# Optimization experiments

Measured on AMD Instinct MI355X. Metric: run time of the kernel, lower is better.

Reference implementation:

```python
import jax, jax.numpy as jnp
import numpy as np

DIM = 1024
NUM_HEADS = 16
HEAD_DIM = DIM // NUM_HEADS


def setup_inputs() -> dict:
    key = jax.random.key(0)
    k_x, k_wqkv, k_bqkv, k_wo, k_bo = jax.random.split(key, 5)
    scale = DIM ** -0.5
    return {
        "x": jax.random.normal(k_x, (4, 2048, DIM), dtype=jnp.float32),
        "w_qkv": jax.random.normal(k_wqkv, (DIM, 3 * DIM), dtype=jnp.float32) * scale,
        "b_qkv": jax.random.normal(k_bqkv, (3 * DIM,), dtype=jnp.float32) * 0.02,
        "w_out": jax.random.normal(k_wo, (DIM, DIM), dtype=jnp.float32) * scale,
        "b_out": jax.random.normal(k_bo, (DIM,), dtype=jnp.float32) * 0.02,
    }


def reference(x, w_qkv, b_qkv, w_out, b_out):
    B, S, D = x.shape
    H, Hd = NUM_HEADS, HEAD_DIM
    # QKV projection: (B,S,3D) -> (3,B,H,S,Hd)
    qkv = (x @ w_qkv + b_qkv).reshape(B, S, 3, H, Hd).transpose(2, 0, 3, 1, 4)
    q, k, v = qkv[0], qkv[1], qkv[2]
    scores = jnp.einsum('bhqd,bhkd->bhqk', q, k) / (Hd ** 0.5)
    attn = jax.nn.softmax(scores, axis=-1)  # dropout is identity in eval
    out = jnp.einsum('bhqk,bhkd->bhqd', attn, v)
    out = out.transpose(0, 2, 1, 3).reshape(B, S, D)
    return out @ w_out + b_out
```

## Files before the change

### kernel.cpp

```cpp
#include <hip/hip_runtime.h>
#include <hip/hip_bf16.h>
#include <stdint.h>

#define SEQ 2048
#define DIM 1024
#define NH 16
#define HD 64

typedef __attribute__((ext_vector_type(8))) short short8;
typedef __attribute__((ext_vector_type(4))) float f32x4;
typedef __attribute__((ext_vector_type(4))) float float4v;
typedef __attribute__((ext_vector_type(4))) unsigned short u16x4;
typedef __attribute__((ext_vector_type(2))) unsigned int u32x2;

#define MFMA16(a, b, c) __builtin_amdgcn_mfma_f32_16x16x32_bf16(a, b, c, 0, 0, 0)

__device__ __forceinline__ unsigned short f2b(float f) {
  union { float f; unsigned int u; } x; x.f = f;
  unsigned int r = (x.u + 0x7FFFu + ((x.u >> 16) & 1u)) >> 16;
  return (unsigned short)r;
}

__device__ __forceinline__ unsigned int pk2(float a, float b) {
  __hip_bfloat162 h = __float22bfloat162_rn(float2{a, b});
  union { __hip_bfloat162 h; unsigned int u; } c; c.h = h;
  return c.u;
}

__device__ __forceinline__ void gld16(const void* g, void* l) {
  __builtin_amdgcn_global_load_lds(
      (const __attribute__((address_space(1))) unsigned int*)(uintptr_t)g,
      (__attribute__((address_space(3))) unsigned int*)(unsigned int)(uintptr_t)l,
      16, 0, 0);
}

__global__ void cast_bf16_kernel(const float* __restrict__ in,
                                 unsigned short* __restrict__ out, int n4) {
  int stride = gridDim.x * blockDim.x;
  for (int i = blockIdx.x * blockDim.x + threadIdx.x; i < n4; i += stride) {
    float4v v = *(const float4v*)(in + (size_t)i * 4);
    u16x4 o;
    o.x = f2b(v.x); o.y = f2b(v.y); o.z = f2b(v.z); o.w = f2b(v.w);
    *(u16x4*)(out + (size_t)i * 4) = o;
  }
}

__global__ void transpose_cast_kernel(const float* __restrict__ in,
                                      unsigned short* __restrict__ out,
                                      int rows, int cols) {
  __shared__ float tile[32][33];
  const int t = threadIdx.x, tx = t & 31, ty = t >> 5;
  const int c0 = blockIdx.x * 32, r0 = blockIdx.y * 32;
#pragma unroll
  for (int j = 0; j < 4; j++)
    tile[ty + 8 * j][tx] = in[(size_t)(r0 + ty + 8 * j) * cols + c0 + tx];
  __syncthreads();
#pragma unroll
  for (int j = 0; j < 4; j++)
    out[(size_t)(c0 + ty + 8 * j) * rows + r0 + tx] = f2b(tile[tx][ty + 8 * j]);
}

template <int EPI>
__global__ __launch_bounds__(256, 2) void gemm_bt_kernel(
    const unsigned short* __restrict__ A, const unsigned short* __restrict__ Bt,
    const float* __restrict__ bias, float* __restrict__ Cf,
    int M, int N, int K,
    unsigned short* __restrict__ Qb, unsigned short* __restrict__ Kb,
    unsigned short* __restrict__ Vt) {
  __shared__ unsigned short lA[128 * 32];
  __shared__ unsigned short lB[128 * 32];
  const int t = threadIdx.x, lane = t & 63, w = t >> 6;
  const int l15 = lane & 15, lg = lane >> 4;
  const int wr = (w >> 1) * 64, wc = (w & 1) * 64;
  const int bm = blockIdx.x, bn = blockIdx.y;
  const char* Ag = (const char*)(A + (size_t)bm * 128 * K);
  const char* Bg = (const char*)(Bt + (size_t)bn * 128 * K);
  const int sr = t >> 2;
  const int sc = (t & 3) * 16;
  const size_t rowb = (size_t)K * 2;

  f32x4 acc[4][4];
#pragma unroll
  for (int m = 0; m < 4; m++)
#pragma unroll
    for (int n = 0; n < 4; n++) acc[m][n] = (f32x4){0.f, 0.f, 0.f, 0.f};

  for (int k0 = 0; k0 < K; k0 += 32) {
    __syncthreads();
    const size_t kbyte = (size_t)k0 * 2;
    gld16(Ag + (size_t)sr * rowb + kbyte + sc, &lA[t * 8]);
    gld16(Ag + (size_t)(sr + 64) * rowb + kbyte + sc, &lA[2048 + t * 8]);
    gld16(Bg + (size_t)sr * rowb + kbyte + sc, &lB[t * 8]);
    gld16(Bg + (size_t)(sr + 64) * rowb + kbyte + sc, &lB[2048 + t * 8]);
    asm volatile("s_waitcnt vmcnt(0)" ::: "memory");
    __syncthreads();
    short8 af[4], bf_[4];
#pragma unroll
    for (int m = 0; m < 4; m++)
      af[m] = *(const short8*)&lA[(wr + m * 16 + l15) * 32 + lg * 8];
#pragma unroll
    for (int n = 0; n < 4; n++)
      bf_[n] = *(const short8*)&lB[(wc + n * 16 + l15) * 32 + lg * 8];
#pragma unroll
    for (int m = 0; m < 4; m++)
#pragma unroll
      for (int n = 0; n < 4; n++)
        acc[m][n] = MFMA16(af[m], bf_[n], acc[m][n]);
  }

#pragma unroll
  for (int m = 0; m < 4; m++) {
#pragma unroll
    for (int n = 0; n < 4; n++) {
      const int row0 = bm * 128 + wr + m * 16 + lg * 4;
      const int col = bn * 128 + wc + n * 16 + l15;
      const float bv = bias[col];
#pragma unroll
      for (int rr = 0; rr < 4; rr++) {
        const float v = acc[m][n][rr] + bv;
        const int row = row0 + rr;
        if (EPI == 1) {
          Cf[(size_t)row * N + col] = v;
        } else {
          const int three = col >> 10, rem = col & 1023;
          const int h = rem >> 6, d = rem & 63;
          const int b = row >> 11, s = row & 2047;
          const size_t bh = (size_t)(b * NH + h);
          if (three == 0)
            Qb[(bh * SEQ + s) * HD + d] = f2b(v * 0.125f);
          else if (three == 1)
            Kb[(bh * SEQ + s) * HD + d] = f2b(v);
          else
            Vt[(bh * HD + d) * SEQ + s] = f2b(v);
        }
      }
    }
  }
}

__global__ __launch_bounds__(256, 4) void attn_kernel(
    const unsigned short* __restrict__ Qb, const unsigned short* __restrict__ Kb,
    const unsigned short* __restrict__ Vt, unsigned short* __restrict__ AO) {
  __shared__ unsigned short kT[2][64 * 64];
  __shared__ unsigned short vT[2][64 * 64];
  __shared__ unsigned short pT[4][16 * 64];
  const int t = threadIdx.x, lane = t & 63, w = t >> 6;
  const int l15 = lane & 15, lg = lane >> 4;
  const int q0 = blockIdx.x * 64;
  const int bh = blockIdx.y;
  const char* Qg = (const char*)(Qb + (size_t)bh * SEQ * HD);
  const char* Kg = (const char*)(Kb + (size_t)bh * SEQ * HD);
  const char* Vg = (const char*)(Vt + (size_t)bh * HD * SEQ);

  short8 qa[2];
  {
    const char* qrow = Qg + (size_t)(q0 + w * 16 + l15) * 128;
    qa[0] = *(const short8*)(qrow + lg * 16);
    qa[1] = *(const short8*)(qrow + 64 + lg * 16);
  }

  f32x4 o[4];
#pragma unroll
  for (int n = 0; n < 4; n++) o[n] = (f32x4){0.f, 0.f, 0.f, 0.f};
  float m_r = -1e30f, l_r = 0.f;

  const int sr0 = t >> 3;
  const int scx = (t & 7) * 16;

#define STAGE(buf, kv0_)                                                               \
  do {                                                                                 \
    const int r0_ = sr0, r1_ = sr0 + 32;                                               \
    gld16(Kg + (size_t)((kv0_) + r0_) * 128 + (scx ^ ((r0_ & 7) << 4)),                \
          &kT[buf][t * 8]);                                                            \
    gld16(Kg + (size_t)((kv0_) + r1_) * 128 + (scx ^ ((r1_ & 7) << 4)),                \
          &kT[buf][2048 + t * 8]);                                                     \
    gld16(Vg + (size_t)r0_ * (SEQ * 2) + (size_t)(kv0_) * 2 + (scx ^ ((r0_ & 7) << 4)),\
          &vT[buf][t * 8]);                                                            \
    gld16(Vg + (size_t)r1_ * (SEQ * 2) + (size_t)(kv0_) * 2 + (scx ^ ((r1_ & 7) << 4)),\
          &vT[buf][2048 + t * 8]);                                                     \
  } while (0)

  STAGE(0, 0);
  asm volatile("s_waitcnt vmcnt(0)" ::: "memory");
  __syncthreads();
  int cur = 0;

  for (int kv0 = 0; kv0 < SEQ; kv0 += 64) {
    if (kv0 + 64 < SEQ) STAGE(cur ^ 1, kv0 + 64);

    const unsigned short* kb = &kT[cur][0];
    f32x4 s[4];
#pragma unroll
    for (int n = 0; n < 4; n++) s[n] = (f32x4){0.f, 0.f, 0.f, 0.f};
    __builtin_amdgcn_s_setprio(1);
#pragma unroll
    for (int n = 0; n < 4; n++) {
      const int row = n * 16 + l15;
      const char* kr = (const char*)kb + row * 128;
      const int sw = (row & 7) << 4;
      short8 a0 = *(const short8*)(kr + ((lg * 16) ^ sw));
      short8 a1 = *(const short8*)(kr + ((64 + lg * 16) ^ sw));
      s[n] = MFMA16(a0, qa[0], s[n]);
      s[n] = MFMA16(a1, qa[1], s[n]);
    }
    __builtin_amdgcn_s_setprio(0);

    float mx = s[0][0];
#pragma unroll
    for (int n = 0; n < 4; n++)
#pragma unroll
      for (int r = 0; r < 4; r++) mx = fmaxf(mx, s[n][r]);
    mx = fmaxf(mx, __shfl_xor(mx, 16, 64));
    mx = fmaxf(mx, __shfl_xor(mx, 32, 64));
    const float nm = fmaxf(m_r, mx);
    const float al = __expf(m_r - nm);
    m_r = nm;
    float rs = 0.f;
#pragma unroll
    for (int n = 0; n < 4; n++)
#pragma unroll
      for (int r = 0; r < 4; r++) {
        const float p = __expf(s[n][r] - nm);
        s[n][r] = p;
        rs += p;
      }
    rs += __shfl_xor(rs, 16, 64);
    rs += __shfl_xor(rs, 32, 64);
    l_r = l_r * al + rs;

    float alb[4];
#pragma unroll
    for (int r = 0; r < 4; r++) alb[r] = __shfl(al, lg * 4 + r, 64);
#pragma unroll
    for (int n = 0; n < 4; n++)
#pragma unroll
      for (int r = 0; r < 4; r++) o[n][r] *= alb[r];

    char* pb = (char*)&pT[w][0];
    const int swp = (l15 & 7) << 4;
#pragma unroll
    for (int n = 0; n < 4; n++) {
      u32x2 c;
      c.x = pk2(s[n][0], s[n][1]);
      c.y = pk2(s[n][2], s[n][3]);
      *(u32x2*)(pb + l15 * 128 + ((n * 32 + lg * 8) ^ swp)) = c;
    }
    short8 pa[2];
    pa[0] = *(const short8*)(pb + l15 * 128 + ((lg * 16) ^ swp));
    pa[1] = *(const short8*)(pb + l15 * 128 + ((64 + lg * 16) ^ swp));

    const unsigned short* vb = &vT[cur][0];
    __builtin_amdgcn_s_setprio(1);
#pragma unroll
    for (int n = 0; n < 4; n++) {
      const int row = n * 16 + l15;
      const char* vr = (const char*)vb + row * 128;
      const int sw = (row & 7) << 4;
      short8 b0 = *(const short8*)(vr + ((lg * 16) ^ sw));
      short8 b1 = *(const short8*)(vr + ((64 + lg * 16) ^ sw));
      o[n] = MFMA16(pa[0], b0, o[n]);
      o[n] = MFMA16(pa[1], b1, o[n]);
    }
    __builtin_amdgcn_s_setprio(0);

    asm volatile("s_waitcnt vmcnt(0)" ::: "memory");
    __syncthreads();
    cur ^= 1;
  }
#undef STAGE

  float lb[4];
#pragma unroll
  for (int r = 0; r < 4; r++) lb[r] = 1.f / __shfl(l_r, lg * 4 + r, 64);
  const int b = bh >> 4, h = bh & 15;
  unsigned short* aob = AO + (size_t)b * SEQ * DIM + (size_t)h * HD;
#pragma unroll
  for (int n = 0; n < 4; n++)
#pragma unroll
    for (int r = 0; r < 4; r++) {
      const int s_ = q0 + w * 16 + lg * 4 + r;
      const int d_ = n * 16 + l15;
      aob[(size_t)s_ * DIM + d_] = f2b(o[n][r] * lb[r]);
    }
}

extern "C" void kernel_launch(void* const* d_in, const int* in_sizes, int n_in,
                              void* d_out, int out_size, void* d_ws, size_t ws_size,
                              hipStream_t stream) {
  const float* x = (const float*)d_in[0];
  const float* w_qkv = (const float*)d_in[1];
  const float* b_qkv = (const float*)d_in[2];
  const float* w_out = (const float*)d_in[3];
  const float* b_out = (const float*)d_in[4];
  float* out = (float*)d_out;

  char* ws = (char*)d_ws;
  unsigned short* xb    = (unsigned short*)(ws);
  unsigned short* wqkvT = (unsigned short*)(ws + (16u << 20));
  unsigned short* woT   = (unsigned short*)(ws + (22u << 20));
  unsigned short* Qb    = (unsigned short*)(ws + (24u << 20));
  unsigned short* Kb    = (unsigned short*)(ws + (40u << 20));
  unsigned short* Vt    = (unsigned short*)(ws + (56u << 20));
  unsigned short* AO    = (unsigned short*)(ws + (72u << 20));

  const int M = 4 * SEQ;

  cast_bf16_kernel<<<2048, 256, 0, stream>>>(x, xb, M * DIM / 4);
  transpose_cast_kernel<<<dim3(3 * DIM / 32, DIM / 32), 256, 0, stream>>>(w_qkv, wqkvT, DIM, 3 * DIM);
  transpose_cast_kernel<<<dim3(DIM / 32, DIM / 32), 256, 0, stream>>>(w_out, woT, DIM, DIM);

  gemm_bt_kernel<0><<<dim3(M / 128, 3 * DIM / 128), 256, 0, stream>>>(
      xb, wqkvT, b_qkv, nullptr, M, 3 * DIM, DIM, Qb, Kb, Vt);

  attn_kernel<<<dim3(SEQ / 64, 4 * NH), 256, 0, stream>>>(Qb, Kb, Vt, AO);

  gemm_bt_kernel<1><<<dim3(M / 128, DIM / 128), 256, 0, stream>>>(
      AO, woT, b_out, out, M, DIM, DIM, nullptr, nullptr, nullptr);
}
```

Before: 332.2 us.

## Process two query tiles per wave and use lazy exp2 softmax rescaling

```diff
diff --git a/kernel.cpp b/kernel.cpp
--- a/kernel.cpp
+++ b/kernel.cpp
@@ -14,6 +14,9 @@
 typedef __attribute__((ext_vector_type(2))) unsigned int u32x2;
 
 #define MFMA16(a, b, c) __builtin_amdgcn_mfma_f32_16x16x32_bf16(a, b, c, 0, 0, 0)
+
+#define QSCALE 0.1803368801111244f
+#define LOG2_THR 11.0f
 
 __device__ __forceinline__ unsigned short f2b(float f) {
   union { float f; unsigned int u; } x; x.f = f;
@@ -127,7 +130,7 @@
           const int b = row >> 11, s = row & 2047;
           const size_t bh = (size_t)(b * NH + h);
           if (three == 0)
-            Qb[(bh * SEQ + s) * HD + d] = f2b(v * 0.125f);
+            Qb[(bh * SEQ + s) * HD + d] = f2b(v * QSCALE);
           else if (three == 1)
             Kb[(bh * SEQ + s) * HD + d] = f2b(v);
           else
@@ -138,31 +141,34 @@
   }
 }
 
-__global__ __launch_bounds__(256, 4) void attn_kernel(
+__global__ __launch_bounds__(256, 3) void attn_kernel(
     const unsigned short* __restrict__ Qb, const unsigned short* __restrict__ Kb,
     const unsigned short* __restrict__ Vt, unsigned short* __restrict__ AO) {
   __shared__ unsigned short kT[2][64 * 64];
   __shared__ unsigned short vT[2][64 * 64];
-  __shared__ unsigned short pT[4][16 * 64];
+  __shared__ unsigned short pT[4][32 * 64];
   const int t = threadIdx.x, lane = t & 63, w = t >> 6;
   const int l15 = lane & 15, lg = lane >> 4;
-  const int q0 = blockIdx.x * 64;
+  const int q0 = blockIdx.x * 128;
   const int bh = blockIdx.y;
   const char* Qg = (const char*)(Qb + (size_t)bh * SEQ * HD);
   const char* Kg = (const char*)(Kb + (size_t)bh * SEQ * HD);
   const char* Vg = (const char*)(Vt + (size_t)bh * HD * SEQ);
 
-  short8 qa[2];
-  {
-    const char* qrow = Qg + (size_t)(q0 + w * 16 + l15) * 128;
-    qa[0] = *(const short8*)(qrow + lg * 16);
-    qa[1] = *(const short8*)(qrow + 64 + lg * 16);
-  }
-
-  f32x4 o[4];
-#pragma unroll
-  for (int n = 0; n < 4; n++) o[n] = (f32x4){0.f, 0.f, 0.f, 0.f};
-  float m_r = -1e30f, l_r = 0.f;
+  short8 qa[2][2];
+#pragma unroll
+  for (int h = 0; h < 2; h++) {
+    const char* qrow = Qg + (size_t)(q0 + w * 32 + h * 16 + l15) * 128;
+    qa[h][0] = *(const short8*)(qrow + lg * 16);
+    qa[h][1] = *(const short8*)(qrow + 64 + lg * 16);
+  }
+
+  f32x4 o[2][4];
+#pragma unroll
+  for (int h = 0; h < 2; h++)
+#pragma unroll
+    for (int n = 0; n < 4; n++) o[h][n] = (f32x4){0.f, 0.f, 0.f, 0.f};
+  float m_r[2] = {-1e30f, -1e30f}, l_r[2] = {0.f, 0.f};
 
   const int sr0 = t >> 3;
   const int scx = (t & 7) * 16;
@@ -188,78 +194,103 @@
   for (int kv0 = 0; kv0 < SEQ; kv0 += 64) {
     if (kv0 + 64 < SEQ) STAGE(cur ^ 1, kv0 + 64);
 
-    const unsigned short* kb = &kT[cur][0];
-    f32x4 s[4];
-#pragma unroll
-    for (int n = 0; n < 4; n++) s[n] = (f32x4){0.f, 0.f, 0.f, 0.f};
+    const char* kb = (const char*)&kT[cur][0];
+    f32x4 s[2][4];
+#pragma unroll
+    for (int h = 0; h < 2; h++)
+#pragma unroll
+      for (int n = 0; n < 4; n++) s[h][n] = (f32x4){0.f, 0.f, 0.f, 0.f};
     __builtin_amdgcn_s_setprio(1);
 #pragma unroll
     for (int n = 0; n < 4; n++) {
       const int row = n * 16 + l15;
-      const char* kr = (const char*)kb + row * 128;
+      const char* kr = kb + row * 128;
       const int sw = (row & 7) << 4;
       short8 a0 = *(const short8*)(kr + ((lg * 16) ^ sw));
       short8 a1 = *(const short8*)(kr + ((64 + lg * 16) ^ sw));
-      s[n] = MFMA16(a0, qa[0], s[n]);
-      s[n] = MFMA16(a1, qa[1], s[n]);
+      s[0][n] = MFMA16(a0, qa[0][0], s[0][n]);
+      s[0][n] = MFMA16(a1, qa[0][1], s[0][n]);
+      s[1][n] = MFMA16(a0, qa[1][0], s[1][n]);
+      s[1][n] = MFMA16(a1, qa[1][1], s[1][n]);
     }
     __builtin_amdgcn_s_setprio(0);
 
-    float mx = s[0][0];
-#pragma unroll
-    for (int n = 0; n < 4; n++)
-#pragma unroll
-      for (int r = 0; r < 4; r++) mx = fmaxf(mx, s[n][r]);
-    mx = fmaxf(mx, __shfl_xor(mx, 16, 64));
-    mx = fmaxf(mx, __shfl_xor(mx, 32, 64));
-    const float nm = fmaxf(m_r, mx);
-    const float al = __expf(m_r - nm);
-    m_r = nm;
-    float rs = 0.f;
-#pragma unroll
-    for (int n = 0; n < 4; n++)
-#pragma unroll
-      for (int r = 0; r < 4; r++) {
-        const float p = __expf(s[n][r] - nm);
-        s[n][r] = p;
-        rs += p;
-      }
-    rs += __shfl_xor(rs, 16, 64);
-    rs += __shfl_xor(rs, 32, 64);
-    l_r = l_r * al + rs;
-
-    float alb[4];
-#pragma unroll
-    for (int r = 0; r < 4; r++) alb[r] = __shfl(al, lg * 4 + r, 64);
-#pragma unroll
-    for (int n = 0; n < 4; n++)
-#pragma unroll
-      for (int r = 0; r < 4; r++) o[n][r] *= alb[r];
+    float mx[2];
+#pragma unroll
+    for (int h = 0; h < 2; h++) {
+      float m0 = fmaxf(fmaxf(s[h][0][0], s[h][0][1]), fmaxf(s[h][0][2], s[h][0][3]));
+#pragma unroll
+      for (int n = 1; n < 4; n++) {
+        m0 = fmaxf(m0, fmaxf(fmaxf(s[h][n][0], s[h][n][1]), fmaxf(s[h][n][2], s[h][n][3])));
+      }
+      m0 = fmaxf(m0, __shfl_xor(m0, 16, 64));
+      m0 = fmaxf(m0, __shfl_xor(m0, 32, 64));
+      mx[h] = m0;
+    }
+
+    const int grow = (mx[0] > m_r[0] + LOG2_THR) | (mx[1] > m_r[1] + LOG2_THR);
+    if (__any(grow)) {
+      float al[2];
+#pragma unroll
+      for (int h = 0; h < 2; h++) {
+        const float nm = fmaxf(m_r[h], mx[h]);
+        al[h] = exp2f(m_r[h] - nm);
+        m_r[h] = nm;
+        l_r[h] *= al[h];
+      }
+#pragma unroll
+      for (int h = 0; h < 2; h++)
+#pragma unroll
+        for (int r = 0; r < 4; r++) {
+          const float alb = __shfl(al[h], lg * 4 + r, 64);
+#pragma unroll
+          for (int n = 0; n < 4; n++) o[h][n][r] *= alb;
+        }
+    }
 
     char* pb = (char*)&pT[w][0];
     const int swp = (l15 & 7) << 4;
 #pragma unroll
-    for (int n = 0; n < 4; n++) {
-      u32x2 c;
-      c.x = pk2(s[n][0], s[n][1]);
-      c.y = pk2(s[n][2], s[n][3]);
-      *(u32x2*)(pb + l15 * 128 + ((n * 32 + lg * 8) ^ swp)) = c;
-    }
-    short8 pa[2];
-    pa[0] = *(const short8*)(pb + l15 * 128 + ((lg * 16) ^ swp));
-    pa[1] = *(const short8*)(pb + l15 * 128 + ((64 + lg * 16) ^ swp));
-
-    const unsigned short* vb = &vT[cur][0];
+    for (int h = 0; h < 2; h++) {
+      float rs = 0.f;
+#pragma unroll
+      for (int n = 0; n < 4; n++) {
+#pragma unroll
+        for (int r = 0; r < 4; r++) {
+          const float p = exp2f(s[h][n][r] - m_r[h]);
+          s[h][n][r] = p;
+          rs += p;
+        }
+        u32x2 c;
+        c.x = pk2(s[h][n][0], s[h][n][1]);
+        c.y = pk2(s[h][n][2], s[h][n][3]);
+        *(u32x2*)(pb + (h * 16 + l15) * 128 + ((n * 32 + lg * 8) ^ swp)) = c;
+      }
+      rs += __shfl_xor(rs, 16, 64);
+      rs += __shfl_xor(rs, 32, 64);
+      l_r[h] += rs;
+    }
+    short8 pa[2][2];
+#pragma unroll
+    for (int h = 0; h < 2; h++) {
+      const char* pr = pb + (h * 16 + l15) * 128;
+      pa[h][0] = *(const short8*)(pr + ((lg * 16) ^ swp));
+      pa[h][1] = *(const short8*)(pr + ((64 + lg * 16) ^ swp));
+    }
+
+    const char* vb = (const char*)&vT[cur][0];
     __builtin_amdgcn_s_setprio(1);
 #pragma unroll
     for (int n = 0; n < 4; n++) {
       const int row = n * 16 + l15;
-      const char* vr = (const char*)vb + row * 128;
+      const char* vr = vb + row * 128;
       const int sw = (row & 7) << 4;
       short8 b0 = *(const short8*)(vr + ((lg * 16) ^ sw));
       short8 b1 = *(const short8*)(vr + ((64 + lg * 16) ^ sw));
-      o[n] = MFMA16(pa[0], b0, o[n]);
-      o[n] = MFMA16(pa[1], b1, o[n]);
+      o[0][n] = MFMA16(pa[0][0], b0, o[0][n]);
+      o[0][n] = MFMA16(pa[0][1], b1, o[0][n]);
+      o[1][n] = MFMA16(pa[1][0], b0, o[1][n]);
+      o[1][n] = MFMA16(pa[1][1], b1, o[1][n]);
     }
     __builtin_amdgcn_s_setprio(0);
 
@@ -269,18 +300,22 @@
   }
 #undef STAGE
 
-  float lb[4];
-#pragma unroll
-  for (int r = 0; r < 4; r++) lb[r] = 1.f / __shfl(l_r, lg * 4 + r, 64);
-  const int b = bh >> 4, h = bh & 15;
-  unsigned short* aob = AO + (size_t)b * SEQ * DIM + (size_t)h * HD;
-#pragma unroll
-  for (int n = 0; n < 4; n++)
+  float inv[2];
+#pragma unroll
+  for (int h = 0; h < 2; h++) inv[h] = 1.f / l_r[h];
+  const int b = bh >> 4, hh = bh & 15;
+  unsigned short* aob = AO + (size_t)b * SEQ * DIM + (size_t)hh * HD;
+#pragma unroll
+  for (int h = 0; h < 2; h++)
 #pragma unroll
     for (int r = 0; r < 4; r++) {
-      const int s_ = q0 + w * 16 + lg * 4 + r;
-      const int d_ = n * 16 + l15;
-      aob[(size_t)s_ * DIM + d_] = f2b(o[n][r] * lb[r]);
+      const float lb = __shfl(inv[h], lg * 4 + r, 64);
+      const int s_ = q0 + w * 32 + h * 16 + lg * 4 + r;
+#pragma unroll
+      for (int n = 0; n < 4; n++) {
+        const int d_ = n * 16 + l15;
+        aob[(size_t)s_ * DIM + d_] = f2b(o[h][n][r] * lb);
+      }
     }
 }
 
@@ -312,7 +347,7 @@
   gemm_bt_kernel<0><<<dim3(M / 128, 3 * DIM / 128), 256, 0, stream>>>(
       xb, wqkvT, b_qkv, nullptr, M, 3 * DIM, DIM, Qb, Kb, Vt);
 
-  attn_kernel<<<dim3(SEQ / 64, 4 * NH), 256, 0, stream>>>(Qb, Kb, Vt, AO);
+  attn_kernel<<<dim3(SEQ / 128, 4 * NH), 256, 0, stream>>>(Qb, Kb, Vt, AO);
 
   gemm_bt_kernel<1><<<dim3(M / 128, DIM / 128), 256, 0, stream>>>(
       AO, woT, b_out, out, M, DIM, DIM, nullptr, nullptr, nullptr);
```

Measured after the change: 329.8 us. About the same (-0.7%).
